# Optimization experiments

Hardware: AMD Instinct MI355X
Metric: run time of the kernel (lower is better)

## Reference

```python
import jax, jax.numpy as jnp
import numpy as np

# Problem dims (see shape_source)
T, H, FFN, K, E = 2048, 1024, 2048, 4, 32
LOCAL_EXPERT_IDS = (0, 8, 16, 24)  # round_robin plan: E=32, ep_size=8, ep_rank=0
N_LOCAL = len(LOCAL_EXPERT_IDS)
W_INIT = 0.02


def setup_inputs() -> dict:
    key = jax.random.key(0)
    k1, k2, k3, k4, k5 = jax.random.split(key, 5)
    hidden_2d = jax.random.normal(k1, (T, H), jnp.float32)
    selected_experts = jax.random.randint(k2, (T, K), 0, E)          # int routing ids
    routing_weights = jax.random.uniform(k3, (T, K), jnp.float32)    # nonneg gate probs
    gate_up_stack = jax.random.normal(k4, (N_LOCAL, 2 * FFN, H), jnp.float32) * W_INIT
    down_stack = jax.random.normal(k5, (N_LOCAL, H, FFN), jnp.float32) * W_INIT
    return {
        "hidden_2d": hidden_2d,
        "selected_experts": selected_experts,
        "routing_weights": routing_weights,
        "gate_up_stack": gate_up_stack,
        "down_stack": down_stack,
    }


def reference(hidden_2d, selected_experts, routing_weights, gate_up_stack, down_stack):
    """JAX port of ShardedExperts.forward_local.

    Same math as the torch sort/gather grouped-GEMM path: for every
    (token, k) assignment whose expert id is local, compute
    down(silu(gate) * up) and scatter-add routing_weight * out into the
    token row. Expressed densely per local expert (fixed small loop),
    which is the jit-friendly equivalent: the per-token expert weight
    w_e[t] = sum_k routing_weights[t,k] * [selected[t,k] == e] collapses
    duplicate assignments exactly like index_add_ does.
    """
    partial = jnp.zeros_like(hidden_2d)
    for i, eid in enumerate(LOCAL_EXPERT_IDS):
        # [T] combined routing weight for this expert (0 for unrouted tokens)
        w_e = jnp.sum(routing_weights * (selected_experts == eid), axis=-1)
        gu = hidden_2d @ gate_up_stack[i].T          # [T, 2*FFN]
        gate, up = jnp.split(gu, 2, axis=-1)         # gu.chunk(2, dim=-1)
        h = jax.nn.silu(gate) * up                   # act_fn(gate) * up
        out = h @ down_stack[i].T                    # [T, H]
        partial = partial + out * w_e[:, None]
    return partial
```

## Files before the change

### kernel.cpp

```cpp
#include <hip/hip_runtime.h>
#include <cstdint>
#include <cstddef>

#define TT  2048
#define HH  1024
#define FFN 2048
#define NL  4
#define BK  64
#define BM  256
#define SK2 2

typedef __attribute__((ext_vector_type(8))) short bf16x8;
typedef __attribute__((ext_vector_type(4))) unsigned short u16x4;
typedef __attribute__((ext_vector_type(4))) float f32x4;

__device__ __forceinline__ unsigned short f2bf(float f) {
  unsigned u = __builtin_bit_cast(unsigned, f);
  u += 0x7FFFu + ((u >> 16) & 1u);
  return (unsigned short)(u >> 16);
}

__device__ __forceinline__ bf16x8 pack8(f32x4 f0, f32x4 f1) {
  bf16x8 v;
  v[0] = (short)f2bf(f0[0]); v[1] = (short)f2bf(f0[1]);
  v[2] = (short)f2bf(f0[2]); v[3] = (short)f2bf(f0[3]);
  v[4] = (short)f2bf(f1[0]); v[5] = (short)f2bf(f1[1]);
  v[6] = (short)f2bf(f1[2]); v[7] = (short)f2bf(f1[3]);
  return v;
}

__device__ __forceinline__ u16x4 pack4(f32x4 f) {
  u16x4 v;
  v[0] = f2bf(f[0]); v[1] = f2bf(f[1]); v[2] = f2bf(f[2]); v[3] = f2bf(f[3]);
  return v;
}

__device__ __forceinline__ void async16(void* lds, const void* g) {
  __builtin_amdgcn_global_load_lds(
      (const __attribute__((address_space(1))) unsigned int*)g,
      (__attribute__((address_space(3))) unsigned int*)lds, 16, 0, 0);
}

__device__ __forceinline__ int swz(int b) { return b ^ (((b >> 7) & 7) << 4); }

__device__ __forceinline__ void lds_barrier() {
  asm volatile("s_waitcnt lgkmcnt(0)" ::: "memory");
  __builtin_amdgcn_s_barrier();
}

__global__ void k_zero(float* __restrict__ out, int* __restrict__ cnt) {
  int i = blockIdx.x * 256 + threadIdx.x;
  f32x4 z = {0.f, 0.f, 0.f, 0.f};
  reinterpret_cast<f32x4*>(out)[i] = z;
  if (i < NL) cnt[i] = 0;
}

__global__ void k_build(const int* __restrict__ sel, const float* __restrict__ rw,
                        int* __restrict__ cnt, int* __restrict__ tok,
                        float* __restrict__ wgt) {
  int t = blockIdx.x * 256 + threadIdx.x;
  if (t >= TT) return;
  int   s0 = sel[t*4+0], s1 = sel[t*4+1], s2 = sel[t*4+2], s3 = sel[t*4+3];
  float r0 = rw[t*4+0],  r1 = rw[t*4+1],  r2 = rw[t*4+2],  r3 = rw[t*4+3];
#pragma unroll
  for (int i = 0; i < NL; ++i) {
    int eid = i * 8;
    float w = 0.f; bool m = false;
    if (s0 == eid) { w += r0; m = true; }
    if (s1 == eid) { w += r1; m = true; }
    if (s2 == eid) { w += r2; m = true; }
    if (s3 == eid) { w += r3; m = true; }
    if (m) {
      int p = atomicAdd(&cnt[i], 1);
      tok[i*TT + p] = t;
      wgt[i*TT + p] = w;
    }
  }
}

__global__ void k_gather(const float* __restrict__ hidden, const int* __restrict__ cnt,
                         const int* __restrict__ tok, unsigned short* __restrict__ X) {
  int p = blockIdx.x, e = blockIdx.y;
  if (p >= cnt[e]) return;
  int t = tok[e*TT + p];
  const f32x4* src = reinterpret_cast<const f32x4*>(hidden + (size_t)t * HH);
  f32x4 a = src[threadIdx.x*2], b = src[threadIdx.x*2 + 1];
  reinterpret_cast<bf16x8*>(X + ((size_t)e*TT + p) * HH)[threadIdx.x] = pack8(a, b);
}

__global__ __launch_bounds__(512) void k_gemm1(
    const unsigned short* __restrict__ X, const float* __restrict__ gup,
    const int* __restrict__ cnt, unsigned short* __restrict__ Hb) {
  int bid = blockIdx.x;
  int xcd = bid & 7;
  int e   = xcd >> 1;
  int idx = (bid >> 3) * 2 + (xcd & 1);
  int n0  = idx * 32;
  int c   = cnt[e];

  __shared__ alignas(16) unsigned short As[4][BM*BK];
  __shared__ alignas(16) unsigned short Bs[2][64*BK];

  int tid  = threadIdx.x;
  int lane = tid & 63, wv = tid >> 6;
  int lr = lane & 15,  lk = lane >> 4;
  int wm = wv >> 1,    wn = wv & 1;

  const unsigned short* Ab = X   + (size_t)e * TT * HH;
  const float*          Gb = gup + (size_t)e * 2 * FFN * HH;

  int arow[4], acol[4], dstA[4];
#pragma unroll
  for (int cc = 0; cc < 4; ++cc) {
    int chunk = wv * 4 + cc;
    int P = chunk * 1024 + lane * 16;
    arow[cc] = P >> 7;
    acol[cc] = (P & 127) ^ ((arow[cc] & 7) << 4);
    dstA[cc] = P;
  }

  int rb  = tid >> 3;
  int cbf = (tid & 7) * 8;
  int grow = (rb < 32) ? (n0 + rb) : (FFN + n0 + rb - 32);
  const float* gB = Gb + (size_t)grow * HH + cbf;
  int wb = swz(rb * 128 + cbf * 2);

  int aoff[4][2], bgo[2], buo[2];
#pragma unroll
  for (int mi = 0; mi < 4; ++mi)
#pragma unroll
    for (int kk = 0; kk < 2; ++kk)
      aoff[mi][kk] = swz((wm*64 + mi*16 + lr) * 128 + kk*64 + lk*16);
#pragma unroll
  for (int kk = 0; kk < 2; ++kk) {
    bgo[kk] = swz((wn*16 + lr) * 128 + kk*64 + lk*16);
    buo[kk] = swz((32 + wn*16 + lr) * 128 + kk*64 + lk*16);
  }

  const int NT = HH / BK;

  for (int m0 = 0; m0 < c; m0 += BM) {
    __syncthreads();

    const char* srcA[4];
#pragma unroll
    for (int cc = 0; cc < 4; ++cc)
      srcA[cc] = (const char*)(Ab + (size_t)(m0 + arow[cc]) * HH) + acol[cc];

    f32x4 accg[4], accu[4];
    f32x4 z = {0.f, 0.f, 0.f, 0.f};
#pragma unroll
    for (int a = 0; a < 4; ++a) { accg[a] = z; accu[a] = z; }

    f32x4 br[3][2];

    br[0][0] = *(const f32x4*)(gB);
    br[0][1] = *(const f32x4*)(gB + 4);
#pragma unroll
    for (int cc = 0; cc < 4; ++cc) async16((char*)As[0] + dstA[cc], srcA[cc]);
#pragma unroll
    for (int cc = 0; cc < 4; ++cc) async16((char*)As[1] + dstA[cc], srcA[cc] + BK*2);
#pragma unroll
    for (int cc = 0; cc < 4; ++cc) async16((char*)As[2] + dstA[cc], srcA[cc] + 2*BK*2);
    br[1][0] = *(const f32x4*)(gB + BK);
    br[1][1] = *(const f32x4*)(gB + BK + 4);
    br[2][0] = *(const f32x4*)(gB + 2*BK);
    br[2][1] = *(const f32x4*)(gB + 2*BK + 4);
    *(bf16x8*)((char*)Bs[0] + wb) = pack8(br[0][0], br[0][1]);
    asm volatile("s_waitcnt vmcnt(12)" ::: "memory");
    lds_barrier();

#pragma unroll
    for (int t = 0; t < NT; ++t) {
      if (t + 3 < NT) {
        int k3 = (t + 3) * BK;
#pragma unroll
        for (int cc = 0; cc < 4; ++cc)
          async16((char*)As[(t+3) & 3] + dstA[cc], srcA[cc] + k3*2);
        br[(t+3) % 3][0] = *(const f32x4*)(gB + k3);
        br[(t+3) % 3][1] = *(const f32x4*)(gB + k3 + 4);
      }
      __builtin_amdgcn_sched_barrier(0);
      {
        const char* Asc = (const char*)As[t & 3];
        const char* Bsc = (const char*)Bs[t & 1];
#pragma unroll
        for (int kk = 0; kk < 2; ++kk) {
          bf16x8 bg = *(const bf16x8*)(Bsc + bgo[kk]);
          bf16x8 bu = *(const bf16x8*)(Bsc + buo[kk]);
#pragma unroll
          for (int mi = 0; mi < 4; ++mi) {
            bf16x8 a = *(const bf16x8*)(Asc + aoff[mi][kk]);
            accg[mi] = __builtin_amdgcn_mfma_f32_16x16x32_bf16(a, bg, accg[mi], 0, 0, 0);
            accu[mi] = __builtin_amdgcn_mfma_f32_16x16x32_bf16(a, bu, accu[mi], 0, 0, 0);
          }
        }
      }
      if (t + 1 < NT) {
        *(bf16x8*)((char*)Bs[(t+1) & 1] + wb) =
            pack8(br[(t+1) % 3][0], br[(t+1) % 3][1]);
        lds_barrier();
      }
    }

#pragma unroll
    for (int mi = 0; mi < 4; ++mi)
#pragma unroll
      for (int j = 0; j < 4; ++j) {
        int p = m0 + wm*64 + mi*16 + lk*4 + j;
        if (p < c) {
          float gv = accg[mi][j];
          float hv = (gv / (1.f + __expf(-gv))) * accu[mi][j];
          Hb[((size_t)e * TT + p) * FFN + (n0 + wn*16 + lr)] = f2bf(hv);
        }
      }
  }
}

__global__ __launch_bounds__(512) void k_gemm2(
    const unsigned short* __restrict__ Hb, const float* __restrict__ down,
    const int* __restrict__ cnt, const int* __restrict__ tok,
    const float* __restrict__ wgt, float* __restrict__ out) {
  int bid = blockIdx.x;
  int xcd = bid & 7;
  int e   = xcd >> 1;
  int sk  = xcd & 1;
  int n0  = (bid >> 3) * 32;
  int c   = cnt[e];
  int kbase = sk * (FFN / SK2);

  __shared__ alignas(16) unsigned short As[4][BM*BK];
  __shared__ alignas(16) unsigned short Bs[2][32*BK];

  int tid  = threadIdx.x;
  int lane = tid & 63, wv = tid >> 6;
  int lr = lane & 15,  lk = lane >> 4;
  int wm = wv >> 1,    wn = wv & 1;

  const unsigned short* Ab = Hb   + (size_t)e * TT * FFN + kbase;
  const float*          Db = down + (size_t)e * HH * FFN;

  int arow[4], acol[4], dstA[4];
#pragma unroll
  for (int cc = 0; cc < 4; ++cc) {
    int chunk = wv * 4 + cc;
    int P = chunk * 1024 + lane * 16;
    arow[cc] = P >> 7;
    acol[cc] = (P & 127) ^ ((arow[cc] & 7) << 4);
    dstA[cc] = P;
  }

  int rb  = tid >> 4;
  int cbf = (tid & 15) * 4;
  const float* gB = Db + (size_t)(n0 + rb) * FFN + kbase + cbf;
  int wb = swz(rb * 128 + cbf * 2);

  int aoff[4][2], boff[2];
#pragma unroll
  for (int mi = 0; mi < 4; ++mi)
#pragma unroll
    for (int kk = 0; kk < 2; ++kk)
      aoff[mi][kk] = swz((wm*64 + mi*16 + lr) * 128 + kk*64 + lk*16);
#pragma unroll
  for (int kk = 0; kk < 2; ++kk)
    boff[kk] = swz((wn*16 + lr) * 128 + kk*64 + lk*16);

  const int NT = (FFN / SK2) / BK;

  for (int m0 = 0; m0 < c; m0 += BM) {
    __syncthreads();

    const char* srcA[4];
#pragma unroll
    for (int cc = 0; cc < 4; ++cc)
      srcA[cc] = (const char*)(Ab + (size_t)(m0 + arow[cc]) * FFN) + acol[cc];

    f32x4 acc[4];
    f32x4 z = {0.f, 0.f, 0.f, 0.f};
#pragma unroll
    for (int a = 0; a < 4; ++a) acc[a] = z;

    f32x4 br[3];

    br[0] = *(const f32x4*)(gB);
#pragma unroll
    for (int cc = 0; cc < 4; ++cc) async16((char*)As[0] + dstA[cc], srcA[cc]);
#pragma unroll
    for (int cc = 0; cc < 4; ++cc) async16((char*)As[1] + dstA[cc], srcA[cc] + BK*2);
#pragma unroll
    for (int cc = 0; cc < 4; ++cc) async16((char*)As[2] + dstA[cc], srcA[cc] + 2*BK*2);
    br[1] = *(const f32x4*)(gB + BK);
    br[2] = *(const f32x4*)(gB + 2*BK);
    *(u16x4*)((char*)Bs[0] + wb) = pack4(br[0]);
    asm volatile("s_waitcnt vmcnt(10)" ::: "memory");
    lds_barrier();

#pragma unroll
    for (int t = 0; t < NT; ++t) {
      if (t + 3 < NT) {
        int k3 = (t + 3) * BK;
#pragma unroll
        for (int cc = 0; cc < 4; ++cc)
          async16((char*)As[(t+3) & 3] + dstA[cc], srcA[cc] + k3*2);
        br[(t+3) % 3] = *(const f32x4*)(gB + k3);
      }
      __builtin_amdgcn_sched_barrier(0);
      {
        const char* Asc = (const char*)As[t & 3];
        const char* Bsc = (const char*)Bs[t & 1];
#pragma unroll
        for (int kk = 0; kk < 2; ++kk) {
          bf16x8 bf_ = *(const bf16x8*)(Bsc + boff[kk]);
#pragma unroll
          for (int mi = 0; mi < 4; ++mi) {
            bf16x8 a = *(const bf16x8*)(Asc + aoff[mi][kk]);
            acc[mi] = __builtin_amdgcn_mfma_f32_16x16x32_bf16(a, bf_, acc[mi], 0, 0, 0);
          }
        }
      }
      if (t + 1 < NT) {
        *(u16x4*)((char*)Bs[(t+1) & 1] + wb) = pack4(br[(t+1) % 3]);
        lds_barrier();
      }
    }

#pragma unroll
    for (int mi = 0; mi < 4; ++mi)
#pragma unroll
      for (int j = 0; j < 4; ++j) {
        int p = m0 + wm*64 + mi*16 + lk*4 + j;
        if (p < c) {
          int   t = tok[e*TT + p];
          float w = wgt[e*TT + p];
          atomicAdd(&out[(size_t)t * HH + (n0 + wn*16 + lr)], w * acc[mi][j]);
        }
      }
  }
}

extern "C" void kernel_launch(void* const* d_in, const int* in_sizes, int n_in,
                              void* d_out, int out_size, void* d_ws, size_t ws_size,
                              hipStream_t stream) {
  const float* hidden = (const float*)d_in[0];
  const int*   sel    = (const int*)d_in[1];
  const float* rw     = (const float*)d_in[2];
  const float* gup    = (const float*)d_in[3];
  const float* dwn    = (const float*)d_in[4];
  float* out = (float*)d_out;

  char* ws = (char*)d_ws;
  int*            cnt  = (int*)ws;
  int*            tok  = (int*)(ws + 1024);
  float*          wgt  = (float*)(ws + 33792);
  unsigned short* X    = (unsigned short*)(ws + 66560);
  unsigned short* Hb   = (unsigned short*)(ws + 16843776);

  k_zero  <<<2048, 256, 0, stream>>>(out, cnt);
  k_build <<<8,    256, 0, stream>>>(sel, rw, cnt, tok, wgt);
  k_gather<<<dim3(TT, NL), 128, 0, stream>>>(hidden, cnt, tok, X);
  k_gemm1 <<<256, 512, 0, stream>>>(X, gup, cnt, Hb);
  k_gemm2 <<<256, 512, 0, stream>>>(Hb, dwn, cnt, tok, wgt, out);
}
```

Before: 55.56 us.

## Stream fp32 down-proj weights to LDS asynchronously and convert to bf16 at use

The down-projection B tile was loaded into registers with global loads, converted to bf16, and written to LDS. It is now copied as raw fp32 into a triple-buffered swizzled LDS area with async global-to-LDS loads, and each wave converts to bf16 after reading its fragment. The intent is to take B loads out of the register/VALU path and pipeline them alongside the A async copies, with explicit vmcnt waits. In exchange, LDS use grows, each wave repeats the fp32-to-bf16 conversion, and the hand-counted waitcnt values must match the number of outstanding copies exactly.

```diff
diff --git a/kernel.cpp b/kernel.cpp
--- a/kernel.cpp
+++ b/kernel.cpp
@@ -230,7 +230,7 @@
   int kbase = sk * (FFN / SK2);
 
   __shared__ alignas(16) unsigned short As[4][BM*BK];
-  __shared__ alignas(16) unsigned short Bs[2][32*BK];
+  __shared__ alignas(16) float          Bf[3][32*BK];
 
   int tid  = threadIdx.x;
   int lane = tid & 63, wv = tid >> 6;
@@ -250,20 +250,25 @@
     dstA[cc] = P;
   }
 
-  int rb  = tid >> 4;
-  int cbf = (tid & 15) * 4;
-  const float* gB = Db + (size_t)(n0 + rb) * FFN + kbase + cbf;
-  int wb = swz(rb * 128 + cbf * 2);
-
-  int aoff[4][2], boff[2];
+  int PB   = wv * 1024 + lane * 16;
+  int rowB = PB >> 8;
+  int colB = (PB & 255) ^ ((rowB & 7) << 4);
+  const char* srcB = (const char*)(Db + (size_t)(n0 + rowB) * FFN + kbase) + colB;
+  int dstB = PB;
+
+  int aoff[4][2], bo0[2], bo1[2];
 #pragma unroll
   for (int mi = 0; mi < 4; ++mi)
 #pragma unroll
     for (int kk = 0; kk < 2; ++kk)
       aoff[mi][kk] = swz((wm*64 + mi*16 + lr) * 128 + kk*64 + lk*16);
 #pragma unroll
-  for (int kk = 0; kk < 2; ++kk)
-    boff[kk] = swz((wn*16 + lr) * 128 + kk*64 + lk*16);
+  for (int kk = 0; kk < 2; ++kk) {
+    int row = wn*16 + lr;
+    int cb  = kk*128 + lk*32;
+    bo0[kk] = row*256 + ((cb)      ^ ((row & 7) << 4));
+    bo1[kk] = row*256 + ((cb + 16) ^ ((row & 7) << 4));
+  }
 
   const int NT = (FFN / SK2) / BK;
 
@@ -280,37 +285,35 @@
 #pragma unroll
     for (int a = 0; a < 4; ++a) acc[a] = z;
 
-    f32x4 br[3];
-
-    br[0] = *(const f32x4*)(gB);
 #pragma unroll
     for (int cc = 0; cc < 4; ++cc) async16((char*)As[0] + dstA[cc], srcA[cc]);
+    async16((char*)Bf[0] + dstB, srcB);
 #pragma unroll
     for (int cc = 0; cc < 4; ++cc) async16((char*)As[1] + dstA[cc], srcA[cc] + BK*2);
+    async16((char*)Bf[1] + dstB, srcB + BK*4);
 #pragma unroll
     for (int cc = 0; cc < 4; ++cc) async16((char*)As[2] + dstA[cc], srcA[cc] + 2*BK*2);
-    br[1] = *(const f32x4*)(gB + BK);
-    br[2] = *(const f32x4*)(gB + 2*BK);
-    *(u16x4*)((char*)Bs[0] + wb) = pack4(br[0]);
-    asm volatile("s_waitcnt vmcnt(10)" ::: "memory");
-    lds_barrier();
+    asm volatile("s_waitcnt vmcnt(9)" ::: "memory");
+    __builtin_amdgcn_s_barrier();
 
 #pragma unroll
     for (int t = 0; t < NT; ++t) {
       if (t + 3 < NT) {
-        int k3 = (t + 3) * BK;
 #pragma unroll
         for (int cc = 0; cc < 4; ++cc)
-          async16((char*)As[(t+3) & 3] + dstA[cc], srcA[cc] + k3*2);
-        br[(t+3) % 3] = *(const f32x4*)(gB + k3);
-      }
+          async16((char*)As[(t+3) & 3] + dstA[cc], srcA[cc] + (t+3)*BK*2);
+      }
+      if (t + 2 < NT)
+        async16((char*)Bf[(t+2) % 3] + dstB, srcB + (size_t)(t+2)*BK*4);
       __builtin_amdgcn_sched_barrier(0);
       {
         const char* Asc = (const char*)As[t & 3];
-        const char* Bsc = (const char*)Bs[t & 1];
+        const char* Bsc = (const char*)Bf[t % 3];
 #pragma unroll
         for (int kk = 0; kk < 2; ++kk) {
-          bf16x8 bf_ = *(const bf16x8*)(Bsc + boff[kk]);
+          f32x4 f0 = *(const f32x4*)(Bsc + bo0[kk]);
+          f32x4 f1 = *(const f32x4*)(Bsc + bo1[kk]);
+          bf16x8 bf_ = pack8(f0, f1);
 #pragma unroll
           for (int mi = 0; mi < 4; ++mi) {
             bf16x8 a = *(const bf16x8*)(Asc + aoff[mi][kk]);
@@ -319,7 +322,9 @@
         }
       }
       if (t + 1 < NT) {
-        *(u16x4*)((char*)Bs[(t+1) & 1] + wb) = pack4(br[(t+1) % 3]);
+        if (t + 3 < NT)      asm volatile("s_waitcnt vmcnt(5)" ::: "memory");
+        else if (t + 2 < NT) asm volatile("s_waitcnt vmcnt(1)" ::: "memory");
+        else                 asm volatile("s_waitcnt vmcnt(0)" ::: "memory");
         lds_barrier();
       }
     }
```

Result: slower. 58.16 us (+4.7%).

## Widen down-proj GEMM N tile to 64 and split K four ways

Applied to the files above, without the earlier changes.

The second GEMM now uses a 64-column output tile per block instead of 32, so each wave computes two 16-wide N fragments and reuses each A fragment for two MFMAs. To keep the block count, the K dimension is split four ways instead of two, and the block index mapping is changed to match. This halves redundant reads of the H activation tile per output column. In exchange it adds more atomic adds into the output and uses more accumulator registers per thread. The B loads become 8-float vectors packed to bf16x8.

```diff
diff --git a/kernel.cpp b/kernel.cpp
--- a/kernel.cpp
+++ b/kernel.cpp
@@ -8,7 +8,7 @@
 #define NL  4
 #define BK  64
 #define BM  256
-#define SK2 2
+#define SK2 4
 
 typedef __attribute__((ext_vector_type(8))) short bf16x8;
 typedef __attribute__((ext_vector_type(4))) unsigned short u16x4;
@@ -26,12 +26,6 @@
   v[2] = (short)f2bf(f0[2]); v[3] = (short)f2bf(f0[3]);
   v[4] = (short)f2bf(f1[0]); v[5] = (short)f2bf(f1[1]);
   v[6] = (short)f2bf(f1[2]); v[7] = (short)f2bf(f1[3]);
-  return v;
-}
-
-__device__ __forceinline__ u16x4 pack4(f32x4 f) {
-  u16x4 v;
-  v[0] = f2bf(f[0]); v[1] = f2bf(f[1]); v[2] = f2bf(f[2]); v[3] = f2bf(f[3]);
   return v;
 }
 
@@ -221,16 +215,17 @@
     const unsigned short* __restrict__ Hb, const float* __restrict__ down,
     const int* __restrict__ cnt, const int* __restrict__ tok,
     const float* __restrict__ wgt, float* __restrict__ out) {
-  int bid = blockIdx.x;
-  int xcd = bid & 7;
-  int e   = xcd >> 1;
-  int sk  = xcd & 1;
-  int n0  = (bid >> 3) * 32;
-  int c   = cnt[e];
+  int bid   = blockIdx.x;
+  int xcd   = bid & 7;
+  int e     = xcd >> 1;
+  int inner = (bid >> 3) * 2 + (xcd & 1);
+  int sk    = inner >> 4;
+  int n0    = (inner & 15) * 64;
+  int c     = cnt[e];
   int kbase = sk * (FFN / SK2);
 
   __shared__ alignas(16) unsigned short As[4][BM*BK];
-  __shared__ alignas(16) unsigned short Bs[2][32*BK];
+  __shared__ alignas(16) unsigned short Bs[2][64*BK];
 
   int tid  = threadIdx.x;
   int lane = tid & 63, wv = tid >> 6;
@@ -250,20 +245,22 @@
     dstA[cc] = P;
   }
 
-  int rb  = tid >> 4;
-  int cbf = (tid & 15) * 4;
+  int rb  = tid >> 3;
+  int cbf = (tid & 7) * 8;
   const float* gB = Db + (size_t)(n0 + rb) * FFN + kbase + cbf;
   int wb = swz(rb * 128 + cbf * 2);
 
-  int aoff[4][2], boff[2];
+  int aoff[4][2], boff[2][2];
 #pragma unroll
   for (int mi = 0; mi < 4; ++mi)
 #pragma unroll
     for (int kk = 0; kk < 2; ++kk)
       aoff[mi][kk] = swz((wm*64 + mi*16 + lr) * 128 + kk*64 + lk*16);
 #pragma unroll
-  for (int kk = 0; kk < 2; ++kk)
-    boff[kk] = swz((wn*16 + lr) * 128 + kk*64 + lk*16);
+  for (int ni = 0; ni < 2; ++ni)
+#pragma unroll
+    for (int kk = 0; kk < 2; ++kk)
+      boff[ni][kk] = swz((wn*32 + ni*16 + lr) * 128 + kk*64 + lk*16);
 
   const int NT = (FFN / SK2) / BK;
 
@@ -275,24 +272,29 @@
     for (int cc = 0; cc < 4; ++cc)
       srcA[cc] = (const char*)(Ab + (size_t)(m0 + arow[cc]) * FFN) + acol[cc];
 
-    f32x4 acc[4];
+    f32x4 acc[4][2];
     f32x4 z = {0.f, 0.f, 0.f, 0.f};
 #pragma unroll
-    for (int a = 0; a < 4; ++a) acc[a] = z;
-
-    f32x4 br[3];
-
-    br[0] = *(const f32x4*)(gB);
+    for (int a = 0; a < 4; ++a)
+#pragma unroll
+      for (int b = 0; b < 2; ++b) acc[a][b] = z;
+
+    f32x4 br[3][2];
+
+    br[0][0] = *(const f32x4*)(gB);
+    br[0][1] = *(const f32x4*)(gB + 4);
 #pragma unroll
     for (int cc = 0; cc < 4; ++cc) async16((char*)As[0] + dstA[cc], srcA[cc]);
 #pragma unroll
     for (int cc = 0; cc < 4; ++cc) async16((char*)As[1] + dstA[cc], srcA[cc] + BK*2);
 #pragma unroll
     for (int cc = 0; cc < 4; ++cc) async16((char*)As[2] + dstA[cc], srcA[cc] + 2*BK*2);
-    br[1] = *(const f32x4*)(gB + BK);
-    br[2] = *(const f32x4*)(gB + 2*BK);
-    *(u16x4*)((char*)Bs[0] + wb) = pack4(br[0]);
-    asm volatile("s_waitcnt vmcnt(10)" ::: "memory");
+    br[1][0] = *(const f32x4*)(gB + BK);
+    br[1][1] = *(const f32x4*)(gB + BK + 4);
+    br[2][0] = *(const f32x4*)(gB + 2*BK);
+    br[2][1] = *(const f32x4*)(gB + 2*BK + 4);
+    *(bf16x8*)((char*)Bs[0] + wb) = pack8(br[0][0], br[0][1]);
+    asm volatile("s_waitcnt vmcnt(12)" ::: "memory");
     lds_barrier();
 
 #pragma unroll
@@ -302,7 +304,8 @@
 #pragma unroll
         for (int cc = 0; cc < 4; ++cc)
           async16((char*)As[(t+3) & 3] + dstA[cc], srcA[cc] + k3*2);
-        br[(t+3) % 3] = *(const f32x4*)(gB + k3);
+        br[(t+3) % 3][0] = *(const f32x4*)(gB + k3);
+        br[(t+3) % 3][1] = *(const f32x4*)(gB + k3 + 4);
       }
       __builtin_amdgcn_sched_barrier(0);
       {
@@ -310,16 +313,19 @@
         const char* Bsc = (const char*)Bs[t & 1];
 #pragma unroll
         for (int kk = 0; kk < 2; ++kk) {
-          bf16x8 bf_ = *(const bf16x8*)(Bsc + boff[kk]);
+          bf16x8 b0 = *(const bf16x8*)(Bsc + boff[0][kk]);
+          bf16x8 b1 = *(const bf16x8*)(Bsc + boff[1][kk]);
 #pragma unroll
           for (int mi = 0; mi < 4; ++mi) {
             bf16x8 a = *(const bf16x8*)(Asc + aoff[mi][kk]);
-            acc[mi] = __builtin_amdgcn_mfma_f32_16x16x32_bf16(a, bf_, acc[mi], 0, 0, 0);
+            acc[mi][0] = __builtin_amdgcn_mfma_f32_16x16x32_bf16(a, b0, acc[mi][0], 0, 0, 0);
+            acc[mi][1] = __builtin_amdgcn_mfma_f32_16x16x32_bf16(a, b1, acc[mi][1], 0, 0, 0);
           }
         }
       }
       if (t + 1 < NT) {
-        *(u16x4*)((char*)Bs[(t+1) & 1] + wb) = pack4(br[(t+1) % 3]);
+        *(bf16x8*)((char*)Bs[(t+1) & 1] + wb) =
+            pack8(br[(t+1) % 3][0], br[(t+1) % 3][1]);
         lds_barrier();
       }
     }
@@ -327,14 +333,17 @@
 #pragma unroll
     for (int mi = 0; mi < 4; ++mi)
 #pragma unroll
-      for (int j = 0; j < 4; ++j) {
-        int p = m0 + wm*64 + mi*16 + lk*4 + j;
-        if (p < c) {
-          int   t = tok[e*TT + p];
-          float w = wgt[e*TT + p];
-          atomicAdd(&out[(size_t)t * HH + (n0 + wn*16 + lr)], w * acc[mi][j]);
+      for (int ni = 0; ni < 2; ++ni)
+#pragma unroll
+        for (int j = 0; j < 4; ++j) {
+          int p = m0 + wm*64 + mi*16 + lk*4 + j;
+          if (p < c) {
+            int   t = tok[e*TT + p];
+            float w = wgt[e*TT + p];
+            atomicAdd(&out[(size_t)t * HH + (n0 + wn*32 + ni*16 + lr)],
+                      w * acc[mi][ni][j]);
+          }
         }
-      }
   }
 }
 
```

Result: slower. 60.97 us (+9.7%).
